# Performance work log

Measured on AMD Instinct MI355X. Metric: run time of the kernel, lower is better.

## Reference

```python
import jax, jax.numpy as jnp
import numpy as np

B, T, N, F, H, E = 8, 16, 10000, 64, 64, 1000000
M = B * N  # flattened node count per timestep
NUM_CLASSES = 3


def setup_inputs() -> dict:
    key = jax.random.key(0)
    ks = jax.random.split(key, 10)
    s = 1.0 / np.sqrt(H)
    return {
        "graph_seq": jax.random.normal(ks[0], (B, T, N, F), dtype=jnp.float32),
        "edge_index_seq": jax.random.randint(ks[1], (T, 2, E), 0, M, dtype=jnp.int32),
        "W_gcn": jax.random.normal(ks[2], (F, H), dtype=jnp.float32) / np.sqrt(F),
        "b_gcn": jnp.zeros((H,), dtype=jnp.float32),
        "W_ih": jax.random.uniform(ks[3], (4 * H, H), jnp.float32, -s, s),
        "W_hh": jax.random.uniform(ks[4], (4 * H, H), jnp.float32, -s, s),
        "b_ih": jax.random.uniform(ks[5], (4 * H,), jnp.float32, -s, s),
        "b_hh": jax.random.uniform(ks[6], (4 * H,), jnp.float32, -s, s),
        "W_fc": jax.random.uniform(ks[7], (NUM_CLASSES, H), jnp.float32, -s, s),
        "b_fc": jax.random.uniform(ks[8], (NUM_CLASSES,), jnp.float32, -s, s),
    }


def _forward(graph_seq, edge_index_seq, W_gcn, b_gcn, W_ih, W_hh, b_ih, b_hh, W_fc, b_fc):
    # GCNConv: x' = D^{-1/2}(A+I)D^{-1/2} (x W) + b, applied on flattened (B*N) nodes per timestep.
    xw = jnp.einsum('btnf,fh->btnh', graph_seq, W_gcn)        # [B,T,N,H]
    xw_t = xw.transpose(1, 0, 2, 3).reshape(T, M, H)          # [T, B*N, H], node index = b*N + n

    def gcn_step(_, inp):
        x, ei = inp                                           # x: [M,H], ei: [2,E]
        src, dst = ei[0], ei[1]
        deg = jax.ops.segment_sum(jnp.ones((E,), x.dtype), dst, num_segments=M) + 1.0  # +1 self loop
        dinv = jax.lax.rsqrt(deg)
        coef = dinv[src] * dinv[dst]                          # [E]
        agg = jax.ops.segment_sum(x[src] * coef[:, None], dst, num_segments=M)
        out = agg + x * (dinv * dinv)[:, None] + b_gcn        # self-loop term + bias
        pooled = out.reshape(B, N, H).mean(axis=1)            # mean over nodes -> [B,H]
        return None, pooled

    _, pooled_seq = jax.lax.scan(gcn_step, None, (xw_t, edge_index_seq))  # [T,B,H]

    def lstm_step(carry, x_t):
        h, c = carry
        z = x_t @ W_ih.T + h @ W_hh.T + b_ih + b_hh           # [B,4H], gate order i,f,g,o
        i, f, g, o = jnp.split(z, 4, axis=-1)
        c = jax.nn.sigmoid(f) * c + jax.nn.sigmoid(i) * jnp.tanh(g)
        h = jax.nn.sigmoid(o) * jnp.tanh(c)
        return (h, c), None

    h0 = jnp.zeros((B, H), dtype=graph_seq.dtype)
    (h_last, _), _ = jax.lax.scan(lstm_step, (h0, h0), pooled_seq)
    return h_last @ W_fc.T + b_fc                             # [B,3]


def reference(graph_seq, edge_index_seq, W_gcn, b_gcn, W_ih, W_hh, b_ih, b_hh, W_fc, b_fc):
    return _forward(graph_seq, edge_index_seq, W_gcn, b_gcn, W_ih, W_hh, b_ih, b_hh, W_fc, b_fc)
```

## Files before the change

kernel.cpp:

```cpp
#include <hip/hip_runtime.h>
#include <hip/hip_bf16.h>

#define BB 8
#define TT 16
#define NNODE 10000
#define FF 64
#define HH 64
#define EE 1000000
#define MM 80000
#define NCLS 3

#define NCHUNK 32
#define NPC 2500
#define CAPB 36032
#define NSEG_H 16
#define HW 20000
#define NSEG_B 32
#define EPW 7816
#define WCAP 144
#define FLUSH_THR 96
#define GPAD 16
#define SPLIT 5
#define RPB 500
#define NCS (NCHUNK * SPLIT)

__global__ __launch_bounds__(256) void k_hist(const int* __restrict__ ei,
                                              unsigned int* __restrict__ part, int t0) {
    __shared__ unsigned int h[HW];
    int seg = blockIdx.x, tloc = blockIdx.y, tg = t0 + tloc;
    for (int i = threadIdx.x; i < HW; i += 256) h[i] = 0u;
    __syncthreads();
    const uint4* dstp = (const uint4*)(ei + (size_t)tg * 2 * EE + EE
                                       + (size_t)seg * (EE / NSEG_H));
    for (int i = threadIdx.x; i < (EE / NSEG_H) / 4; i += 256) {
        uint4 d4 = dstp[i];
        atomicAdd(&h[d4.x >> 2], 1u << ((d4.x & 3u) * 8u));
        atomicAdd(&h[d4.y >> 2], 1u << ((d4.y & 3u) * 8u));
        atomicAdd(&h[d4.z >> 2], 1u << ((d4.z & 3u) * 8u));
        atomicAdd(&h[d4.w >> 2], 1u << ((d4.w & 3u) * 8u));
    }
    __syncthreads();
    unsigned int* outp = part + ((size_t)tloc * NSEG_H + seg) * HW;
    for (int i = threadIdx.x; i < HW; i += 256) outp[i] = h[i];
}

__global__ __launch_bounds__(256) void k_mdeg(const unsigned int* __restrict__ part,
                                              float* __restrict__ dinv) {
    int w = blockIdx.x * 256 + threadIdx.x;
    int tloc = blockIdx.y;
    if (w >= HW) return;
    const unsigned int* p = part + (size_t)tloc * NSEG_H * HW;
    unsigned int s = 0;
#pragma unroll
    for (int k = 0; k < NSEG_H; k++) s += p[(size_t)k * HW + w];
    float4 r;
    r.x = rsqrtf((float)(s & 255u) + 1.0f);
    r.y = rsqrtf((float)((s >> 8) & 255u) + 1.0f);
    r.z = rsqrtf((float)((s >> 16) & 255u) + 1.0f);
    r.w = rsqrtf((float)((s >> 24) & 255u) + 1.0f);
    *(float4*)(dinv + (size_t)tloc * MM + (size_t)w * 4) = r;
}

__global__ __launch_bounds__(256) void k_part(const int* __restrict__ ei,
                                              unsigned int* __restrict__ buck,
                                              unsigned int* __restrict__ gcur, int t0) {
    __shared__ unsigned int stg[4][NCHUNK][WCAP];
    __shared__ unsigned int cur[4][NCHUNK];
    int wave = threadIdx.x >> 6, lane = threadIdx.x & 63;
    int tloc = blockIdx.y, tg = t0 + tloc;
    if (lane < NCHUNK) cur[wave][lane] = 0u;

    int wseg = blockIdx.x * 4 + wave;
    int e0 = wseg * EPW;
    int e1 = e0 + EPW; if (e1 > EE) e1 = EE;
    const uint4* src4 = (const uint4*)(ei + (size_t)tg * 2 * EE);
    const uint4* dst4 = (const uint4*)(ei + (size_t)tg * 2 * EE + EE);
    unsigned int* gc = gcur + (size_t)tloc * NCHUNK * GPAD;
    unsigned int* bk = buck + (size_t)tloc * NCHUNK * CAPB;

    int i40 = e0 >> 2, i41 = e1 >> 2;
    int nIter = (i41 - i40 + 63) >> 6;
    for (int k = 0; k < nIter; k++) {
        int i4 = i40 + k * 64 + lane;
        if (i4 < i41) {
            uint4 s4 = src4[i4];
            uint4 d4 = dst4[i4];
            unsigned int ss[4] = {s4.x, s4.y, s4.z, s4.w};
            unsigned int dd[4] = {d4.x, d4.y, d4.z, d4.w};
#pragma unroll
            for (int j = 0; j < 4; j++) {
                unsigned int ck = (unsigned int)(((unsigned long long)ss[j] * 1717987ull) >> 32);
                unsigned int so = ss[j] - ck * NPC;
                unsigned int p = atomicAdd(&cur[wave][ck], 1u);
                if (p < WCAP) stg[wave][ck][p] = (so << 17) | dd[j];
            }
        }
        unsigned int cnt = (lane < NCHUNK) ? cur[wave][lane] : 0u;
        unsigned long long mask = __ballot(cnt >= FLUSH_THR);
        while (mask) {
            int ck = __ffsll((unsigned long long)mask) - 1;
            mask &= mask - 1;
            unsigned int n = cur[wave][ck];
            if (n > WCAP) n = WCAP;
            unsigned int gp = 0;
            if (lane == 0) gp = atomicAdd(&gc[ck * GPAD], n);
            gp = (unsigned int)__shfl((int)gp, 0);
            if (gp + n <= CAPB) {
                for (unsigned int j = lane; j < n; j += 64)
                    bk[(size_t)ck * CAPB + gp + j] = stg[wave][ck][j];
            }
            if (lane == 0) cur[wave][ck] = 0u;
        }
    }
    for (int ck = 0; ck < NCHUNK; ck++) {
        unsigned int n = cur[wave][ck];
        if (n > WCAP) n = WCAP;
        if (n > 0u) {
            unsigned int gp = 0;
            if (lane == 0) gp = atomicAdd(&gc[ck * GPAD], n);
            gp = (unsigned int)__shfl((int)gp, 0);
            if (gp + n <= CAPB) {
                for (unsigned int j = lane; j < n; j += 64)
                    bk[(size_t)ck * CAPB + gp + j] = stg[wave][ck][j];
            }
        }
    }
}

__global__ __launch_bounds__(512) void k_build(const float* __restrict__ dinv,
                                               const unsigned int* __restrict__ buck,
                                               const unsigned int* __restrict__ gcur,
                                               float* __restrict__ ag, int t0) {
    __shared__ float a[NPC * BB];
    int c = blockIdx.x, tloc = blockIdx.y;
    for (int i = threadIdx.x; i < NPC * BB; i += 512) a[i] = 0.0f;
    __syncthreads();

    const float* dv = dinv + (size_t)tloc * MM;
    unsigned int n = gcur[((size_t)tloc * NCHUNK + c) * GPAD];
    if (n > CAPB) n = CAPB;
    const unsigned int* bk = buck + ((size_t)tloc * NCHUNK + c) * CAPB;

    unsigned int n4 = n >> 2;
    for (unsigned int i = threadIdx.x; i < n4; i += 512) {
        uint4 r = ((const uint4*)bk)[i];
        unsigned int rec[4] = {r.x, r.y, r.z, r.w};
#pragma unroll
        for (int k = 0; k < 4; k++) {
            unsigned int d = rec[k] & 0x1FFFFu;
            unsigned int so = rec[k] >> 17;
            unsigned int b = (unsigned int)(((unsigned long long)d * 429497ull) >> 32);
            atomicAdd(&a[so * BB + b], dv[d]);
        }
    }
    {
        unsigned int i = (n4 << 2) + threadIdx.x;
        if (i < n) {
            unsigned int rec = bk[i];
            unsigned int d = rec & 0x1FFFFu;
            unsigned int so = rec >> 17;
            unsigned int b = (unsigned int)(((unsigned long long)d * 429497ull) >> 32);
            atomicAdd(&a[so * BB + b], dv[d]);
        }
    }
    __syncthreads();

    float4* agp = (float4*)(ag + ((size_t)tloc * NCHUNK + c) * NPC * BB);
    for (int i = threadIdx.x; i < NPC * BB / 4; i += 512)
        agp[i] = ((const float4*)a)[i];
}

__global__ __launch_bounds__(256) void k_red(const float* __restrict__ g,
                                             const float* __restrict__ dinv,
                                             const float* __restrict__ ag,
                                             float* __restrict__ yp, int t0) {
    __shared__ float as_[RPB * BB];
    __shared__ float dvs[RPB];
    int u = blockIdx.x;
    int c = u / SPLIT, s = u - c * SPLIT;
    int tloc = blockIdx.y, tg = t0 + tloc;

    const float* agp = ag + (((size_t)tloc * NCHUNK + c) * NPC + (size_t)s * RPB) * BB;
    for (int i = threadIdx.x; i < RPB * BB / 4; i += 256)
        ((float4*)as_)[i] = ((const float4*)agp)[i];
    const float* dvp = dinv + (size_t)tloc * MM + c * NPC + s * RPB;
    for (int i = threadIdx.x; i < RPB; i += 256) dvs[i] = dvp[i];
    __syncthreads();

    int lane = threadIdx.x & 63;
    int wave = threadIdx.x >> 6;
    int sub = lane >> 4;
    int f0 = (lane & 15) << 2;
    int b_c = c >> 2;
    const size_t base_g = ((size_t)(b_c * TT + tg) * NNODE
                           + (size_t)(c & 3) * NPC + (size_t)s * RPB) * FF;

    float acc[BB][4];
#pragma unroll
    for (int b = 0; b < BB; b++)
#pragma unroll
        for (int q = 0; q < 4; q++) acc[b][q] = 0.0f;

    const int NG = RPB / 4;
    for (int gi = wave; gi < NG; gi += 8) {
        int j0 = gi * 4 + sub;
        int gi1 = gi + 4;
        int j1 = gi1 * 4 + sub;
        bool has1 = (gi1 < NG);
        const float4 g40 = *(const float4*)(g + base_g + (size_t)j0 * FF + f0);
        float4 g41 = has1 ? *(const float4*)(g + base_g + (size_t)j1 * FF + f0)
                          : make_float4(0.f, 0.f, 0.f, 0.f);
        {
            float dvj = dvs[j0];
            const float4 a0 = *(const float4*)(&as_[j0 * BB]);
            const float4 a1 = *(const float4*)(&as_[j0 * BB + 4]);
            float av[BB] = {a0.x, a0.y, a0.z, a0.w, a1.x, a1.y, a1.z, a1.w};
#pragma unroll
            for (int b = 0; b < BB; b++) {
                float wv = dvj * (av[b] + (b == b_c ? dvj : 0.0f));
                acc[b][0] = fmaf(g40.x, wv, acc[b][0]);
                acc[b][1] = fmaf(g40.y, wv, acc[b][1]);
                acc[b][2] = fmaf(g40.z, wv, acc[b][2]);
                acc[b][3] = fmaf(g40.w, wv, acc[b][3]);
            }
        }
        if (has1) {
            float dvj = dvs[j1];
            const float4 a0 = *(const float4*)(&as_[j1 * BB]);
            const float4 a1 = *(const float4*)(&as_[j1 * BB + 4]);
            float av[BB] = {a0.x, a0.y, a0.z, a0.w, a1.x, a1.y, a1.z, a1.w};
#pragma unroll
            for (int b = 0; b < BB; b++) {
                float wv = dvj * (av[b] + (b == b_c ? dvj : 0.0f));
                acc[b][0] = fmaf(g41.x, wv, acc[b][0]);
                acc[b][1] = fmaf(g41.y, wv, acc[b][1]);
                acc[b][2] = fmaf(g41.z, wv, acc[b][2]);
                acc[b][3] = fmaf(g41.w, wv, acc[b][3]);
            }
        }
    }

    __syncthreads();
#pragma unroll
    for (int b = 0; b < BB; b++)
#pragma unroll
        for (int q = 0; q < 4; q++) {
            float v = acc[b][q];
            v += __shfl_xor(v, 16);
            v += __shfl_xor(v, 32);
            acc[b][q] = v;
        }
    if (sub == 0) {
#pragma unroll
        for (int b = 0; b < BB; b++)
#pragma unroll
            for (int q = 0; q < 4; q++)
                as_[wave * (BB * FF) + b * FF + f0 + q] = acc[b][q];
    }
    __syncthreads();
    for (int idx = threadIdx.x; idx < BB * FF; idx += 256) {
        float sv = as_[idx] + as_[BB * FF + idx] + as_[2 * BB * FF + idx] + as_[3 * BB * FF + idx];
        yp[((size_t)tg * NCS + u) * (BB * FF) + idx] = sv;
    }
}

__global__ __launch_bounds__(256) void k_lstm(const float* __restrict__ yp,
                                              const float* __restrict__ Wg,
                                              const float* __restrict__ bg,
                                              const float* __restrict__ Wih,
                                              const float* __restrict__ Whh,
                                              const float* __restrict__ bih,
                                              const float* __restrict__ bhh,
                                              const float* __restrict__ Wfc,
                                              const float* __restrict__ bfc,
                                              float* __restrict__ out) {
    int b = blockIdx.x;
    int r = threadIdx.x;

    __shared__ float ys[TT][FF];
    __shared__ float xs[TT][HH];
    __shared__ float hs[HH], cs[HH], zs[4 * HH];

    for (int idx = r; idx < TT * FF; idx += 256) {
        int t = idx >> 6, f = idx & 63;
        const float* p = yp + (size_t)t * NCS * BB * FF + b * FF + f;
        float s = 0.0f;
#pragma unroll 8
        for (int u = 0; u < NCS; u++) s += p[(size_t)u * BB * FF];
        ys[t][f] = s;
    }
    __syncthreads();

    for (int idx = r; idx < TT * HH; idx += 256) {
        int t = idx >> 6, h = idx & 63;
        float s = 0.0f;
#pragma unroll
        for (int f = 0; f < FF; f++) s = fmaf(ys[t][f], Wg[f * HH + h], s);
        xs[t][h] = s * (1.0f / NNODE) + bg[h];
    }

    float wih[HH], whh[HH];
#pragma unroll
    for (int k = 0; k < HH; k++) {
        wih[k] = Wih[r * HH + k];
        whh[k] = Whh[r * HH + k];
    }
    float bias = bih[r] + bhh[r];

    if (r < HH) { hs[r] = 0.0f; cs[r] = 0.0f; }
    __syncthreads();

    for (int t = 0; t < TT; t++) {
        float acc = bias;
#pragma unroll
        for (int k = 0; k < HH; k++)
            acc = fmaf(wih[k], xs[t][k], fmaf(whh[k], hs[k], acc));
        zs[r] = acc;
        __syncthreads();
        if (r < HH) {
            float iv = zs[r], fv = zs[HH + r], gv = zs[2 * HH + r], ov = zs[3 * HH + r];
            float si = 1.0f / (1.0f + expf(-iv));
            float sf = 1.0f / (1.0f + expf(-fv));
            float so = 1.0f / (1.0f + expf(-ov));
            float cc = sf * cs[r] + si * tanhf(gv);
            cs[r] = cc;
            hs[r] = so * tanhf(cc);
        }
        __syncthreads();
    }

    if (r < NCLS) {
        float s = bfc[r];
#pragma unroll
        for (int k = 0; k < HH; k++) s = fmaf(hs[k], Wfc[r * HH + k], s);
        out[b * NCLS + r] = s;
    }
}

extern "C" void kernel_launch(void* const* d_in, const int* in_sizes, int n_in,
                              void* d_out, int out_size, void* d_ws, size_t ws_size,
                              hipStream_t stream) {
    const float* g   = (const float*)d_in[0];
    const int*   ei  = (const int*)d_in[1];
    const float* Wg  = (const float*)d_in[2];
    const float* bg  = (const float*)d_in[3];
    const float* Wih = (const float*)d_in[4];
    const float* Whh = (const float*)d_in[5];
    const float* bih = (const float*)d_in[6];
    const float* bhh = (const float*)d_in[7];
    const float* Wfc = (const float*)d_in[8];
    const float* bfc = (const float*)d_in[9];
    float* out = (float*)d_out;

    char* ws = (char*)d_ws;
    float* yp = (float*)ws;
    const size_t ypBytes = (size_t)TT * NCS * BB * FF * sizeof(float);

    const size_t sz_dinv = (size_t)MM * 4;
    const size_t sz_part = (size_t)NSEG_H * HW * 4;
    const size_t sz_buck = (size_t)NCHUNK * CAPB * 4;
    const size_t sz_gcur = (size_t)NCHUNK * GPAD * 4;
    const size_t sz_ag   = (size_t)NCHUNK * NPC * BB * 4;
    const size_t per_t = sz_dinv + sz_part + sz_buck + sz_gcur + sz_ag;

    size_t avail = (ws_size > ypBytes) ? ws_size - ypBytes : 0;
    int Tg = (int)(avail / per_t);
    if (Tg > TT) Tg = TT;
    if (Tg < 1) Tg = 1;

    size_t ofs = ypBytes;
    float* dinv        = (float*)(ws + ofs); ofs += (size_t)Tg * sz_dinv;
    unsigned int* part = (unsigned int*)(ws + ofs); ofs += (size_t)Tg * sz_part;
    unsigned int* buck = (unsigned int*)(ws + ofs); ofs += (size_t)Tg * sz_buck;
    unsigned int* gcur = (unsigned int*)(ws + ofs); ofs += (size_t)Tg * sz_gcur;
    float* ag          = (float*)(ws + ofs);

    for (int t0 = 0; t0 < TT; t0 += Tg) {
        int tc = (TT - t0 < Tg) ? (TT - t0) : Tg;
        hipMemsetAsync(gcur, 0, (size_t)tc * NCHUNK * GPAD * 4, stream);

        dim3 gh(NSEG_H, tc);
        k_hist<<<gh, 256, 0, stream>>>(ei, part, t0);

        dim3 gm((HW + 255) / 256, tc);
        k_mdeg<<<gm, 256, 0, stream>>>(part, dinv);

        dim3 gp(NSEG_B, tc);
        k_part<<<gp, 256, 0, stream>>>(ei, buck, gcur, t0);

        dim3 gb(NCHUNK, tc);
        k_build<<<gb, 512, 0, stream>>>(dinv, buck, gcur, ag, t0);

        dim3 gr(NCS, tc);
        k_red<<<gr, 256, 0, stream>>>(g, dinv, ag, yp, t0);
    }

    k_lstm<<<BB, 256, 0, stream>>>(yp, Wg, bg, Wih, Whh, bih, bhh, Wfc, bfc, out);
}
```

Baseline: 379.0 us.

## Store packed byte degrees, use rsqrt LUT, rechunk sources, fold partials separately

The packed 8-bit degree counts are now stored directly instead of expanded float dinv. k_build looks up rsqrt through a 256-entry shared LUT indexed by degree byte, and k_red recomputes rsqrt on the fly. That cuts dinv write and gather traffic. The gcur memset moves into k_mdeg, and the source partitioning changes to 40 chunks of 2000 nodes with 4-way split. A new k_fold kernel reduces the partial sums so the LSTM kernel no longer does the serial per-batch reduction. This relies on per-node degree fitting in a byte, as the code before already assumed.

```diff
diff --git a/kernel.cpp b/kernel.cpp
--- a/kernel.cpp
+++ b/kernel.cpp
@@ -10,17 +10,17 @@
 #define MM 80000
 #define NCLS 3
 
-#define NCHUNK 32
-#define NPC 2500
-#define CAPB 36032
+#define NCHUNK 40
+#define NPC 2000
+#define CAPB 26048
 #define NSEG_H 16
 #define HW 20000
 #define NSEG_B 32
 #define EPW 7816
-#define WCAP 144
-#define FLUSH_THR 96
+#define WCAP 96
+#define FLUSH_THR 64
 #define GPAD 16
-#define SPLIT 5
+#define SPLIT 4
 #define RPB 500
 #define NCS (NCHUNK * SPLIT)
 
@@ -45,20 +45,18 @@
 }
 
 __global__ __launch_bounds__(256) void k_mdeg(const unsigned int* __restrict__ part,
-                                              float* __restrict__ dinv) {
+                                              unsigned int* __restrict__ degb,
+                                              unsigned int* __restrict__ gcur) {
+    int tloc = blockIdx.y;
+    if (blockIdx.x == 0 && threadIdx.x < NCHUNK)
+        gcur[((size_t)tloc * NCHUNK + threadIdx.x) * GPAD] = 0u;
     int w = blockIdx.x * 256 + threadIdx.x;
-    int tloc = blockIdx.y;
     if (w >= HW) return;
     const unsigned int* p = part + (size_t)tloc * NSEG_H * HW;
     unsigned int s = 0;
 #pragma unroll
     for (int k = 0; k < NSEG_H; k++) s += p[(size_t)k * HW + w];
-    float4 r;
-    r.x = rsqrtf((float)(s & 255u) + 1.0f);
-    r.y = rsqrtf((float)((s >> 8) & 255u) + 1.0f);
-    r.z = rsqrtf((float)((s >> 16) & 255u) + 1.0f);
-    r.w = rsqrtf((float)((s >> 24) & 255u) + 1.0f);
-    *(float4*)(dinv + (size_t)tloc * MM + (size_t)w * 4) = r;
+    degb[(size_t)tloc * HW + w] = s;
 }
 
 __global__ __launch_bounds__(256) void k_part(const int* __restrict__ ei,
@@ -89,7 +87,7 @@
             unsigned int dd[4] = {d4.x, d4.y, d4.z, d4.w};
 #pragma unroll
             for (int j = 0; j < 4; j++) {
-                unsigned int ck = (unsigned int)(((unsigned long long)ss[j] * 1717987ull) >> 32);
+                unsigned int ck = (unsigned int)(((unsigned long long)ss[j] * 2147484ull) >> 32);
                 unsigned int so = ss[j] - ck * NPC;
                 unsigned int p = atomicAdd(&cur[wave][ck], 1u);
                 if (p < WCAP) stg[wave][ck][p] = (so << 17) | dd[j];
@@ -127,16 +125,18 @@
     }
 }
 
-__global__ __launch_bounds__(512) void k_build(const float* __restrict__ dinv,
+__global__ __launch_bounds__(512) void k_build(const unsigned int* __restrict__ degb,
                                                const unsigned int* __restrict__ buck,
                                                const unsigned int* __restrict__ gcur,
                                                float* __restrict__ ag, int t0) {
     __shared__ float a[NPC * BB];
+    __shared__ float lut[256];
     int c = blockIdx.x, tloc = blockIdx.y;
     for (int i = threadIdx.x; i < NPC * BB; i += 512) a[i] = 0.0f;
-    __syncthreads();
-
-    const float* dv = dinv + (size_t)tloc * MM;
+    if (threadIdx.x < 256) lut[threadIdx.x] = rsqrtf((float)threadIdx.x + 1.0f);
+    __syncthreads();
+
+    const unsigned char* degc = (const unsigned char*)(degb + (size_t)tloc * HW);
     unsigned int n = gcur[((size_t)tloc * NCHUNK + c) * GPAD];
     if (n > CAPB) n = CAPB;
     const unsigned int* bk = buck + ((size_t)tloc * NCHUNK + c) * CAPB;
@@ -150,7 +150,7 @@
             unsigned int d = rec[k] & 0x1FFFFu;
             unsigned int so = rec[k] >> 17;
             unsigned int b = (unsigned int)(((unsigned long long)d * 429497ull) >> 32);
-            atomicAdd(&a[so * BB + b], dv[d]);
+            atomicAdd(&a[so * BB + b], lut[degc[d]]);
         }
     }
     {
@@ -160,7 +160,7 @@
             unsigned int d = rec & 0x1FFFFu;
             unsigned int so = rec >> 17;
             unsigned int b = (unsigned int)(((unsigned long long)d * 429497ull) >> 32);
-            atomicAdd(&a[so * BB + b], dv[d]);
+            atomicAdd(&a[so * BB + b], lut[degc[d]]);
         }
     }
     __syncthreads();
@@ -171,29 +171,32 @@
 }
 
 __global__ __launch_bounds__(256) void k_red(const float* __restrict__ g,
-                                             const float* __restrict__ dinv,
+                                             const unsigned int* __restrict__ degb,
                                              const float* __restrict__ ag,
                                              float* __restrict__ yp, int t0) {
     __shared__ float as_[RPB * BB];
     __shared__ float dvs[RPB];
     int u = blockIdx.x;
-    int c = u / SPLIT, s = u - c * SPLIT;
+    int c = u >> 2, s = u & 3;
     int tloc = blockIdx.y, tg = t0 + tloc;
 
     const float* agp = ag + (((size_t)tloc * NCHUNK + c) * NPC + (size_t)s * RPB) * BB;
     for (int i = threadIdx.x; i < RPB * BB / 4; i += 256)
         ((float4*)as_)[i] = ((const float4*)agp)[i];
-    const float* dvp = dinv + (size_t)tloc * MM + c * NPC + s * RPB;
-    for (int i = threadIdx.x; i < RPB; i += 256) dvs[i] = dvp[i];
+    const unsigned char* degc = (const unsigned char*)(degb + (size_t)tloc * HW)
+                                + c * NPC + s * RPB;
+    for (int i = threadIdx.x; i < RPB; i += 256)
+        dvs[i] = rsqrtf((float)degc[i] + 1.0f);
     __syncthreads();
 
     int lane = threadIdx.x & 63;
     int wave = threadIdx.x >> 6;
     int sub = lane >> 4;
     int f0 = (lane & 15) << 2;
-    int b_c = c >> 2;
+    int b_c = c / 5;
+    int coff = c - b_c * 5;
     const size_t base_g = ((size_t)(b_c * TT + tg) * NNODE
-                           + (size_t)(c & 3) * NPC + (size_t)s * RPB) * FF;
+                           + (size_t)coff * NPC + (size_t)s * RPB) * FF;
 
     float acc[BB][4];
 #pragma unroll
@@ -264,7 +267,18 @@
     }
 }
 
-__global__ __launch_bounds__(256) void k_lstm(const float* __restrict__ yp,
+__global__ __launch_bounds__(512) void k_fold(const float* __restrict__ yp,
+                                              float* __restrict__ y2) {
+    int t = blockIdx.x;
+    int idx = threadIdx.x;
+    const float* p = yp + (size_t)t * NCS * BB * FF + idx;
+    float s = 0.0f;
+#pragma unroll 8
+    for (int u = 0; u < NCS; u++) s += p[(size_t)u * BB * FF];
+    y2[(size_t)t * BB * FF + idx] = s;
+}
+
+__global__ __launch_bounds__(256) void k_lstm(const float* __restrict__ y2,
                                               const float* __restrict__ Wg,
                                               const float* __restrict__ bg,
                                               const float* __restrict__ Wih,
@@ -277,25 +291,15 @@
     int b = blockIdx.x;
     int r = threadIdx.x;
 
-    __shared__ float ys[TT][FF];
     __shared__ float xs[TT][HH];
     __shared__ float hs[HH], cs[HH], zs[4 * HH];
 
-    for (int idx = r; idx < TT * FF; idx += 256) {
-        int t = idx >> 6, f = idx & 63;
-        const float* p = yp + (size_t)t * NCS * BB * FF + b * FF + f;
-        float s = 0.0f;
-#pragma unroll 8
-        for (int u = 0; u < NCS; u++) s += p[(size_t)u * BB * FF];
-        ys[t][f] = s;
-    }
-    __syncthreads();
-
     for (int idx = r; idx < TT * HH; idx += 256) {
         int t = idx >> 6, h = idx & 63;
+        const float* yt = y2 + ((size_t)t * BB + b) * FF;
         float s = 0.0f;
 #pragma unroll
-        for (int f = 0; f < FF; f++) s = fmaf(ys[t][f], Wg[f * HH + h], s);
+        for (int f = 0; f < FF; f++) s = fmaf(yt[f], Wg[f * HH + h], s);
         xs[t][h] = s * (1.0f / NNODE) + bg[h];
     }
 
@@ -355,45 +359,48 @@
     char* ws = (char*)d_ws;
     float* yp = (float*)ws;
     const size_t ypBytes = (size_t)TT * NCS * BB * FF * sizeof(float);
-
-    const size_t sz_dinv = (size_t)MM * 4;
+    float* y2 = (float*)(ws + ypBytes);
+    const size_t y2Bytes = (size_t)TT * BB * FF * sizeof(float);
+    const size_t headBytes = ypBytes + y2Bytes;
+
     const size_t sz_part = (size_t)NSEG_H * HW * 4;
+    const size_t sz_degb = (size_t)HW * 4;
     const size_t sz_buck = (size_t)NCHUNK * CAPB * 4;
     const size_t sz_gcur = (size_t)NCHUNK * GPAD * 4;
     const size_t sz_ag   = (size_t)NCHUNK * NPC * BB * 4;
-    const size_t per_t = sz_dinv + sz_part + sz_buck + sz_gcur + sz_ag;
-
-    size_t avail = (ws_size > ypBytes) ? ws_size - ypBytes : 0;
+    const size_t per_t = sz_part + sz_degb + sz_buck + sz_gcur + sz_ag;
+
+    size_t avail = (ws_size > headBytes) ? ws_size - headBytes : 0;
     int Tg = (int)(avail / per_t);
     if (Tg > TT) Tg = TT;
     if (Tg < 1) Tg = 1;
 
-    size_t ofs = ypBytes;
-    float* dinv        = (float*)(ws + ofs); ofs += (size_t)Tg * sz_dinv;
+    size_t ofs = headBytes;
     unsigned int* part = (unsigned int*)(ws + ofs); ofs += (size_t)Tg * sz_part;
+    unsigned int* degb = (unsigned int*)(ws + ofs); ofs += (size_t)Tg * sz_degb;
     unsigned int* buck = (unsigned int*)(ws + ofs); ofs += (size_t)Tg * sz_buck;
     unsigned int* gcur = (unsigned int*)(ws + ofs); ofs += (size_t)Tg * sz_gcur;
     float* ag          = (float*)(ws + ofs);
 
     for (int t0 = 0; t0 < TT; t0 += Tg) {
         int tc = (TT - t0 < Tg) ? (TT - t0) : Tg;
-        hipMemsetAsync(gcur, 0, (size_t)tc * NCHUNK * GPAD * 4, stream);
 
         dim3 gh(NSEG_H, tc);
         k_hist<<<gh, 256, 0, stream>>>(ei, part, t0);
 
         dim3 gm((HW + 255) / 256, tc);
-        k_mdeg<<<gm, 256, 0, stream>>>(part, dinv);
+        k_mdeg<<<gm, 256, 0, stream>>>(part, degb, gcur);
 
         dim3 gp(NSEG_B, tc);
         k_part<<<gp, 256, 0, stream>>>(ei, buck, gcur, t0);
 
         dim3 gb(NCHUNK, tc);
-        k_build<<<gb, 512, 0, stream>>>(dinv, buck, gcur, ag, t0);
+        k_build<<<gb, 512, 0, stream>>>(degb, buck, gcur, ag, t0);
 
         dim3 gr(NCS, tc);
-        k_red<<<gr, 256, 0, stream>>>(g, dinv, ag, yp, t0);
-    }
-
-    k_lstm<<<BB, 256, 0, stream>>>(yp, Wg, bg, Wih, Whh, bih, bhh, Wfc, bfc, out);
-}
+        k_red<<<gr, 256, 0, stream>>>(g, degb, ag, yp, t0);
+    }
+
+    k_fold<<<TT, 512, 0, stream>>>(yp, y2);
+    k_lstm<<<BB, 256, 0, stream>>>(y2, Wg, bg, Wih, Whh, bih, bhh, Wfc, bfc, out);
+}
```

Measured after the change: 390.0 us. 2.9% more time.
